# Kernel optimization log

Measured on AMD Instinct MI355X. Metric: run time of the kernel, lower is better.

## Reference

```python
import jax, jax.numpy as jnp
import numpy as np

H = 1024      # hidden_size
I = 2 * H     # intermediate_size (expand_factor=2)
N = 16        # ssm_state_size
K = 4         # conv_kernel
BATCH = 2
SEQ = 2048


def setup_inputs() -> dict:
    key = jax.random.key(0)
    k = jax.random.split(key, 6)
    x = jax.random.normal(k[0], (BATCH, SEQ, H), dtype=jnp.float32)
    # nn.Linear default init ~ U(-1/sqrt(fan_in), 1/sqrt(fan_in)); scale is fine for a reference
    W_in = jax.random.normal(k[1], (2 * I, H), dtype=jnp.float32) / np.sqrt(H)
    conv_w = jax.random.normal(k[2], (I, 1, K), dtype=jnp.float32) / np.sqrt(K)
    W_x = jax.random.normal(k[3], (2 * N + 1, I), dtype=jnp.float32) / np.sqrt(I)
    A_log = jax.random.normal(k[4], (I, N), dtype=jnp.float32)
    D = jnp.ones((I,), dtype=jnp.float32)
    W_out = jax.random.normal(k[5], (H, I), dtype=jnp.float32) / np.sqrt(I)
    return {"x": x, "W_in": W_in, "conv_w": conv_w, "W_x": W_x,
            "A_log": A_log, "D": D, "W_out": W_out}


def reference(x, W_in, conv_w, W_x, A_log, D, W_out):
    xz = jnp.einsum('bsh,ih->bsi', x, W_in)
    xp, z = jnp.split(xz, 2, axis=-1)
    # depthwise causal conv1d: pad left K-1 (torch pads both sides then slices [:S])
    xc = jax.lax.conv_general_dilated(
        xp.transpose(0, 2, 1),           # (B, I, S)
        conv_w,                          # (I, 1, K) = OIH with groups=I
        window_strides=(1,),
        padding=[(K - 1, 0)],
        feature_group_count=I,
        dimension_numbers=('NCH', 'OIH', 'NCH'),
    ).transpose(0, 2, 1)                 # (B, S, I)
    xc = jax.nn.silu(xc)
    # x_proj -> delta (1), B (N), C (N)
    xproj = jnp.einsum('bsi,pi->bsp', xc, W_x)   # (B,S,2N+1)
    delta = jax.nn.softplus(xproj[..., :1])       # (B,S,1)
    Bmat = xproj[..., 1:1 + N]                    # (B,S,N)
    Cmat = xproj[..., 1 + N:]                     # (B,S,N)
    A = -jnp.exp(A_log)                           # (I,N)
    # decay/states broadcast-reduce: (B,S,I,N) intermediates reduced over N
    decay = jnp.exp(delta[..., None] * A[None, None])            # (B,S,I,N)
    states = xc[..., None] * Bmat[:, :, None, :] * decay          # (B,S,I,N)
    y = jnp.sum(states * Cmat[:, :, None, :], axis=-1)            # (B,S,I)
    y = y + xc * D[None, None, :]
    return jnp.einsum('bsi,hi->bsh', y * jax.nn.silu(z), W_out)
```

## Files before the change

kernel.cpp:

```cpp
#include <hip/hip_runtime.h>

#define LOG2E 1.4426950408889634f

__device__ __forceinline__ float b2f(unsigned short u) {
    unsigned int v = ((unsigned int)u) << 16;
    return __builtin_bit_cast(float, v);
}
__device__ __forceinline__ unsigned short f2b(float f) {
    unsigned int u = __builtin_bit_cast(unsigned int, f);
    u += 0x7fffu + ((u >> 16) & 1u);
    return (unsigned short)(u >> 16);
}
__device__ __forceinline__ float fexp(float x) {
    return __builtin_amdgcn_exp2f(x * LOG2E);
}
__device__ __forceinline__ float silu_f(float x) {
    return x * __builtin_amdgcn_rcpf(1.0f + fexp(-x));
}

typedef const __attribute__((address_space(1))) unsigned int* gas_t;
typedef __attribute__((address_space(3))) unsigned int* las_t;
__device__ __forceinline__ void gl2lds16(const unsigned short* g, unsigned short* l) {
    __builtin_amdgcn_global_load_lds((gas_t)(const void*)g, (las_t)(void*)l, 16, 0, 0);
}

__global__ __launch_bounds__(256) void cvt_all_k(const float* __restrict__ x,
                                                 const float* __restrict__ W_in,
                                                 const float* __restrict__ W_out,
                                                 const float* __restrict__ W_x,
                                                 unsigned short* __restrict__ xb,
                                                 unsigned short* __restrict__ wib,
                                                 unsigned short* __restrict__ wob,
                                                 unsigned short* __restrict__ wxb) {
    int b = blockIdx.x;
    const float* src;
    unsigned short* dst;
    if (b < 4096)       { src = x;     dst = xb;  }
    else if (b < 8192)  { src = W_in;  dst = wib; b -= 4096; }
    else if (b < 10240) { src = W_out; dst = wob; b -= 8192; }
    else                { src = W_x;   dst = wxb; b -= 10240; }
    int i = b * 256 + threadIdx.x;
    float4 v = ((const float4*)src)[i];
    *(ushort4*)(dst + (size_t)i * 4) = make_ushort4(f2b(v.x), f2b(v.y), f2b(v.z), f2b(v.w));
}

typedef __bf16 bf16x8 __attribute__((ext_vector_type(8)));
typedef float  fx4    __attribute__((ext_vector_type(4)));
typedef int    ix4    __attribute__((ext_vector_type(4)));
union FragU { ix4 i; bf16x8 b; };

template <bool OUT_BF16>
__global__ __launch_bounds__(256) void gemm_bt(const unsigned short* __restrict__ A,
                                               const unsigned short* __restrict__ B,
                                               void* __restrict__ C, int N, int K) {
    __shared__ __align__(16) unsigned short sA[128 * 64];
    __shared__ __align__(16) unsigned short sB[128 * 64];
    const int tid  = threadIdx.x;
    const int lane = tid & 63, wave = tid >> 6;
    const int bm = blockIdx.y * 128, bn = blockIdx.x * 128;
    const int wm = (wave >> 1) * 64, wn = (wave & 1) * 64;
    const int row16 = lane & 15, quad = lane >> 4;
    const int srow = lane >> 3;
    const int sc16 = (lane & 7) ^ srow;
    const unsigned short* gA = A + (size_t)(bm + wave * 32 + srow) * K + sc16 * 8;
    const unsigned short* gB = B + (size_t)(bn + wave * 32 + srow) * K + sc16 * 8;
    unsigned short* lA = sA + (wave * 4) * 512;
    unsigned short* lB = sB + (wave * 4) * 512;
    fx4 acc[4][4] = {};

    for (int kt = 0; kt < K; kt += 64) {
#pragma unroll
        for (int it = 0; it < 4; ++it) {
            gl2lds16(gA + (size_t)it * 8 * K + kt, lA + it * 512);
            gl2lds16(gB + (size_t)it * 8 * K + kt, lB + it * 512);
        }
        __syncthreads();
#pragma unroll
        for (int kk = 0; kk < 64; kk += 32) {
            FragU af[4], bf[4];
#pragma unroll
            for (int t = 0; t < 4; ++t) {
                int ra = wm + t * 16 + row16;
                af[t].i = *(const ix4*)(sA + ra * 64 + ((quad + (kk >> 3)) ^ (ra & 7)) * 8);
            }
#pragma unroll
            for (int t = 0; t < 4; ++t) {
                int rb = wn + t * 16 + row16;
                bf[t].i = *(const ix4*)(sB + rb * 64 + ((quad + (kk >> 3)) ^ (rb & 7)) * 8);
            }
#pragma unroll
            for (int tm = 0; tm < 4; ++tm)
#pragma unroll
                for (int tn = 0; tn < 4; ++tn)
                    acc[tm][tn] = __builtin_amdgcn_mfma_f32_16x16x32_bf16(
                        af[tm].b, bf[tn].b, acc[tm][tn], 0, 0, 0);
        }
        __syncthreads();
    }
#pragma unroll
    for (int tm = 0; tm < 4; ++tm) {
        int row0 = bm + wm + tm * 16 + quad * 4;
#pragma unroll
        for (int tn = 0; tn < 4; ++tn) {
            int col = bn + wn + tn * 16 + row16;
#pragma unroll
            for (int r = 0; r < 4; ++r) {
                float v = acc[tm][tn][r];
                if (OUT_BF16)
                    ((unsigned short*)C)[(size_t)(row0 + r) * N + col] = f2b(v);
                else
                    ((float*)C)[(size_t)(row0 + r) * N + col] = v;
            }
        }
    }
}

__global__ __launch_bounds__(256) void gemm_bt_n64(const unsigned short* __restrict__ A,
                                                   const unsigned short* __restrict__ B,
                                                   float* __restrict__ C, int N, int K) {
    __shared__ __align__(16) unsigned short sA[128 * 64];
    __shared__ __align__(16) unsigned short sB[64 * 64];
    const int tid  = threadIdx.x;
    const int lane = tid & 63, wave = tid >> 6;
    const int bm = blockIdx.y * 128, bn = blockIdx.x * 64;
    const int wm = wave * 32;
    const int row16 = lane & 15, quad = lane >> 4;
    const int srow = lane >> 3;
    const int sc16 = (lane & 7) ^ srow;
    const unsigned short* gA = A + (size_t)(bm + wave * 32 + srow) * K + sc16 * 8;
    const unsigned short* gB = B + (size_t)(bn + wave * 16 + srow) * K + sc16 * 8;
    unsigned short* lA = sA + (wave * 4) * 512;
    unsigned short* lB = sB + (wave * 2) * 512;
    fx4 acc[2][4] = {};

    for (int kt = 0; kt < K; kt += 64) {
#pragma unroll
        for (int it = 0; it < 4; ++it)
            gl2lds16(gA + (size_t)it * 8 * K + kt, lA + it * 512);
#pragma unroll
        for (int it = 0; it < 2; ++it)
            gl2lds16(gB + (size_t)it * 8 * K + kt, lB + it * 512);
        __syncthreads();
#pragma unroll
        for (int kk = 0; kk < 64; kk += 32) {
            FragU af[2], bf[4];
#pragma unroll
            for (int t = 0; t < 2; ++t) {
                int ra = wm + t * 16 + row16;
                af[t].i = *(const ix4*)(sA + ra * 64 + ((quad + (kk >> 3)) ^ (ra & 7)) * 8);
            }
#pragma unroll
            for (int t = 0; t < 4; ++t) {
                int rb = t * 16 + row16;
                bf[t].i = *(const ix4*)(sB + rb * 64 + ((quad + (kk >> 3)) ^ (rb & 7)) * 8);
            }
#pragma unroll
            for (int tm = 0; tm < 2; ++tm)
#pragma unroll
                for (int tn = 0; tn < 4; ++tn)
                    acc[tm][tn] = __builtin_amdgcn_mfma_f32_16x16x32_bf16(
                        af[tm].b, bf[tn].b, acc[tm][tn], 0, 0, 0);
        }
        __syncthreads();
    }
#pragma unroll
    for (int tm = 0; tm < 2; ++tm) {
        int row0 = bm + wm + tm * 16 + quad * 4;
#pragma unroll
        for (int tn = 0; tn < 4; ++tn) {
            int col = bn + tn * 16 + row16;
#pragma unroll
            for (int r = 0; r < 4; ++r)
                C[(size_t)(row0 + r) * N + col] = acc[tm][tn][r];
        }
    }
}

__global__ __launch_bounds__(256) void conv_silu_k(const unsigned short* __restrict__ xz,
                                                   const float* __restrict__ cw,
                                                   unsigned short* __restrict__ xcb) {
    const int ti = threadIdx.x & 31, tm = threadIdx.x >> 5;
    const int i0 = blockIdx.x * 256 + ti * 8;
    const int m  = blockIdx.y * 8 + tm;
    const int s  = m & 2047;
    float w[8][4];
    const float4* cw4 = (const float4*)cw;
#pragma unroll
    for (int j = 0; j < 8; ++j) {
        float4 t = cw4[i0 + j];
        w[j][0] = t.x; w[j][1] = t.y; w[j][2] = t.z; w[j][3] = t.w;
    }
    float acc[8] = {0, 0, 0, 0, 0, 0, 0, 0};
#pragma unroll
    for (int k = 0; k < 4; ++k) {
        int sr = s - 3 + k;
        if (sr >= 0) {
            const unsigned short* p = xz + (size_t)(m - 3 + k) * 4096 + i0;
            ushort4 a = *(const ushort4*)p;
            ushort4 b = *(const ushort4*)(p + 4);
            float v[8] = {b2f(a.x), b2f(a.y), b2f(a.z), b2f(a.w),
                          b2f(b.x), b2f(b.y), b2f(b.z), b2f(b.w)};
#pragma unroll
            for (int j = 0; j < 8; ++j) acc[j] += v[j] * w[j][k];
        }
    }
    unsigned short* qb = xcb + (size_t)m * 2048 + i0;
    *(ushort4*)qb       = make_ushort4(f2b(silu_f(acc[0])), f2b(silu_f(acc[1])),
                                       f2b(silu_f(acc[2])), f2b(silu_f(acc[3])));
    *(ushort4*)(qb + 4) = make_ushort4(f2b(silu_f(acc[4])), f2b(silu_f(acc[5])),
                                       f2b(silu_f(acc[6])), f2b(silu_f(acc[7])));
}

__global__ __launch_bounds__(256) void xproj_mfma(const unsigned short* __restrict__ xcb,
                                                  const unsigned short* __restrict__ wxb,
                                                  float* __restrict__ dg) {
    __shared__ float sX[4][16][49];
    const int tid = threadIdx.x;
    const int lane = tid & 63, wave = tid >> 6;
    const int row16 = lane & 15, quad = lane >> 4;
    const int m0 = blockIdx.x * 16;
    fx4 acc[3] = {};
    const unsigned short* ap = xcb + (size_t)(m0 + row16) * 2048 + wave * 512 + quad * 8;
    const unsigned short* bp = wxb + (size_t)row16 * 2048 + wave * 512 + quad * 8;
#pragma unroll 4
    for (int kk = 0; kk < 512; kk += 32) {
        FragU a, b0, b1, b2;
        a.i  = *(const ix4*)(ap + kk);
        b0.i = *(const ix4*)(bp + kk);
        b1.i = *(const ix4*)(bp + 16 * 2048 + kk);
        b2.i = *(const ix4*)(bp + 32 * 2048 + kk);
        acc[0] = __builtin_amdgcn_mfma_f32_16x16x32_bf16(a.b, b0.b, acc[0], 0, 0, 0);
        acc[1] = __builtin_amdgcn_mfma_f32_16x16x32_bf16(a.b, b1.b, acc[1], 0, 0, 0);
        acc[2] = __builtin_amdgcn_mfma_f32_16x16x32_bf16(a.b, b2.b, acc[2], 0, 0, 0);
    }
#pragma unroll
    for (int t = 0; t < 3; ++t)
#pragma unroll
        for (int r = 0; r < 4; ++r)
            sX[wave][quad * 4 + r][t * 16 + row16] = acc[t][r];
    __syncthreads();
    for (int idx = tid; idx < 272; idx += 256) {
        int rr = idx / 17, q = idx - rr * 17;
        float o;
        if (q == 0) {
            float v = sX[0][rr][0] + sX[1][rr][0] + sX[2][rr][0] + sX[3][rr][0];
            o = (v > 20.f) ? v : log1pf(fexp(v));
        } else {
            float bs = sX[0][rr][q]      + sX[1][rr][q]      + sX[2][rr][q]      + sX[3][rr][q];
            float cs = sX[0][rr][q + 16] + sX[1][rr][q + 16] + sX[2][rr][q + 16] + sX[3][rr][q + 16];
            o = bs * cs;
        }
        dg[(size_t)(m0 + rr) * 17 + q] = o;
    }
}

__global__ __launch_bounds__(256) void ssm_pw_k(const unsigned short* __restrict__ xz,
                                                const unsigned short* __restrict__ xcb,
                                                const float* __restrict__ dg,
                                                const float* __restrict__ Alog,
                                                const float* __restrict__ Dv,
                                                unsigned short* __restrict__ y2) {
    __shared__ float sa[64 * 19];
    __shared__ float sdg[32 * 17];
    const int tid = threadIdx.x;
    const int bi = blockIdx.x, bm = blockIdx.y;
    for (int t = tid; t < 1024; t += 256) {
        float a = Alog[bi * 1024 + t];
        int il = t >> 4, n = t & 15;
        sa[il * 19 + n] = -fexp(a) * LOG2E;
    }
    for (int t = tid; t < 544; t += 256) sdg[t] = dg[(size_t)bm * 32 * 17 + t];
    __syncthreads();
    const int t_i = tid & 7, t_m = tid >> 3;
    const int m  = bm * 32 + t_m;
    const int i0 = bi * 64 + t_i * 8;
    const float delta = sdg[t_m * 17];
    float G[16];
#pragma unroll
    for (int n = 0; n < 16; ++n) G[n] = sdg[t_m * 17 + 1 + n];
    const unsigned short* xcp = xcb + (size_t)m * 2048 + i0;
    ushort4 xu0 = *(const ushort4*)xcp, xu1 = *(const ushort4*)(xcp + 4);
    const unsigned short* zp = xz + (size_t)m * 4096 + 2048 + i0;
    ushort4 zu0 = *(const ushort4*)zp, zu1 = *(const ushort4*)(zp + 4);
    float4 d0 = *(const float4*)(Dv + i0), d1 = *(const float4*)(Dv + i0 + 4);
    float xcv[8] = {b2f(xu0.x), b2f(xu0.y), b2f(xu0.z), b2f(xu0.w),
                    b2f(xu1.x), b2f(xu1.y), b2f(xu1.z), b2f(xu1.w)};
    float zv[8]  = {b2f(zu0.x), b2f(zu0.y), b2f(zu0.z), b2f(zu0.w),
                    b2f(zu1.x), b2f(zu1.y), b2f(zu1.z), b2f(zu1.w)};
    float dv[8]  = {d0.x, d0.y, d0.z, d0.w, d1.x, d1.y, d1.z, d1.w};
    unsigned short outv[8];
#pragma unroll
    for (int ii = 0; ii < 8; ++ii) {
        const float* ap = sa + (t_i * 8 + ii) * 19;
        float ssum = 0.f;
#pragma unroll
        for (int n = 0; n < 16; ++n)
            ssum += G[n] * __builtin_amdgcn_exp2f(delta * ap[n]);
        float y = xcv[ii] * (dv[ii] + ssum);
        outv[ii] = f2b(y * silu_f(zv[ii]));
    }
    unsigned short* q = y2 + (size_t)m * 2048 + i0;
    *(ushort4*)q       = make_ushort4(outv[0], outv[1], outv[2], outv[3]);
    *(ushort4*)(q + 4) = make_ushort4(outv[4], outv[5], outv[6], outv[7]);
}

extern "C" void kernel_launch(void* const* d_in, const int* in_sizes, int n_in,
                              void* d_out, int out_size, void* d_ws, size_t ws_size,
                              hipStream_t stream) {
    const float* x      = (const float*)d_in[0];
    const float* W_in   = (const float*)d_in[1];
    const float* conv_w = (const float*)d_in[2];
    const float* W_x    = (const float*)d_in[3];
    const float* A_log  = (const float*)d_in[4];
    const float* Dvec   = (const float*)d_in[5];
    const float* W_out  = (const float*)d_in[6];

    char* ws = (char*)d_ws;
    unsigned short* xb  = (unsigned short*)(ws);
    unsigned short* wib = (unsigned short*)(ws + 8388608);
    unsigned short* wob = (unsigned short*)(ws + 16777216);
    unsigned short* xz  = (unsigned short*)(ws + 20971520);
    float*          dgp = (float*)        (ws + 54525952);
    unsigned short* y2  = (unsigned short*)(ws + 54804480);
    unsigned short* xcb = (unsigned short*)(ws + 71581696);
    unsigned short* wxb = (unsigned short*)(ws + 88358912);

    cvt_all_k<<<10306, 256, 0, stream>>>(x, W_in, W_out, W_x, xb, wib, wob, wxb);
    gemm_bt<true><<<dim3(32, 32), 256, 0, stream>>>(xb, wib, xz, 4096, 1024);
    conv_silu_k<<<dim3(8, 512), 256, 0, stream>>>(xz, conv_w, xcb);
    xproj_mfma<<<256, 256, 0, stream>>>(xcb, wxb, dgp);
    ssm_pw_k<<<dim3(32, 128), 256, 0, stream>>>(xz, xcb, dgp, A_log, Dvec, y2);
    gemm_bt_n64<<<dim3(16, 32), 256, 0, stream>>>(y2, wob, (float*)d_out, 1024, 2048);
}
```

Before: 233.1 us.

## Fuse conv+silu, x_proj and SSM pointwise into one kernel via LDS

Merges the three middle kernels into one block-per-16-rows kernel that keeps the conv/silu output in swizzled shared memory, runs the x_proj MFMA from LDS, and computes the SSM pointwise output directly. This removes the global round trips for xc and the delta/G buffer and two kernel launches. In exchange, each block now recomputes exp(A_log) for all 2048 channels, and only 256 blocks with 64KB+ of LDS each run, which reduces parallelism and occupancy in the exp-heavy SSM stage.

```diff
diff --git a/kernel.cpp b/kernel.cpp
--- a/kernel.cpp
+++ b/kernel.cpp
@@ -176,68 +176,74 @@
     }
 }
 
-__global__ __launch_bounds__(256) void conv_silu_k(const unsigned short* __restrict__ xz,
+__global__ __launch_bounds__(256) void fused_mid_k(const unsigned short* __restrict__ xz,
                                                    const float* __restrict__ cw,
-                                                   unsigned short* __restrict__ xcb) {
-    const int ti = threadIdx.x & 31, tm = threadIdx.x >> 5;
-    const int i0 = blockIdx.x * 256 + ti * 8;
-    const int m  = blockIdx.y * 8 + tm;
-    const int s  = m & 2047;
-    float w[8][4];
-    const float4* cw4 = (const float4*)cw;
-#pragma unroll
-    for (int j = 0; j < 8; ++j) {
-        float4 t = cw4[i0 + j];
-        w[j][0] = t.x; w[j][1] = t.y; w[j][2] = t.z; w[j][3] = t.w;
-    }
-    float acc[8] = {0, 0, 0, 0, 0, 0, 0, 0};
-#pragma unroll
-    for (int k = 0; k < 4; ++k) {
-        int sr = s - 3 + k;
-        if (sr >= 0) {
-            const unsigned short* p = xz + (size_t)(m - 3 + k) * 4096 + i0;
-            ushort4 a = *(const ushort4*)p;
-            ushort4 b = *(const ushort4*)(p + 4);
-            float v[8] = {b2f(a.x), b2f(a.y), b2f(a.z), b2f(a.w),
-                          b2f(b.x), b2f(b.y), b2f(b.z), b2f(b.w)};
-#pragma unroll
-            for (int j = 0; j < 8; ++j) acc[j] += v[j] * w[j][k];
-        }
-    }
-    unsigned short* qb = xcb + (size_t)m * 2048 + i0;
-    *(ushort4*)qb       = make_ushort4(f2b(silu_f(acc[0])), f2b(silu_f(acc[1])),
-                                       f2b(silu_f(acc[2])), f2b(silu_f(acc[3])));
-    *(ushort4*)(qb + 4) = make_ushort4(f2b(silu_f(acc[4])), f2b(silu_f(acc[5])),
-                                       f2b(silu_f(acc[6])), f2b(silu_f(acc[7])));
-}
-
-__global__ __launch_bounds__(256) void xproj_mfma(const unsigned short* __restrict__ xcb,
-                                                  const unsigned short* __restrict__ wxb,
-                                                  float* __restrict__ dg) {
+                                                   const unsigned short* __restrict__ wxb,
+                                                   const float* __restrict__ Alog,
+                                                   const float* __restrict__ Dv,
+                                                   unsigned short* __restrict__ y2) {
+    __shared__ __align__(16) unsigned short sxc[16 * 2048];
     __shared__ float sX[4][16][49];
-    const int tid = threadIdx.x;
+    __shared__ float sdg[16 * 17];
+    const int tid  = threadIdx.x;
     const int lane = tid & 63, wave = tid >> 6;
     const int row16 = lane & 15, quad = lane >> 4;
     const int m0 = blockIdx.x * 16;
-    fx4 acc[3] = {};
-    const unsigned short* ap = xcb + (size_t)(m0 + row16) * 2048 + wave * 512 + quad * 8;
-    const unsigned short* bp = wxb + (size_t)row16 * 2048 + wave * 512 + quad * 8;
+
+    {
+        const float4* cw4 = (const float4*)cw;
+        float w[8][4];
+#pragma unroll
+        for (int c = 0; c < 8; ++c) {
+            float4 t4 = cw4[tid * 8 + c];
+            w[c][0] = t4.x; w[c][1] = t4.y; w[c][2] = t4.z; w[c][3] = t4.w;
+        }
+        for (int j = 0; j < 16; ++j) {
+            const int m = m0 + j, s = m & 2047;
+            float acc[8] = {0, 0, 0, 0, 0, 0, 0, 0};
+#pragma unroll
+            for (int k = 0; k < 4; ++k) {
+                if (s - 3 + k >= 0) {
+                    const unsigned short* p = xz + (size_t)(m - 3 + k) * 4096 + tid * 8;
+                    ushort4 a = *(const ushort4*)p;
+                    ushort4 b = *(const ushort4*)(p + 4);
+                    float v[8] = {b2f(a.x), b2f(a.y), b2f(a.z), b2f(a.w),
+                                  b2f(b.x), b2f(b.y), b2f(b.z), b2f(b.w)};
+#pragma unroll
+                    for (int c = 0; c < 8; ++c) acc[c] += v[c] * w[c][k];
+                }
+            }
+            unsigned short* q = sxc + j * 2048 + ((tid ^ (j & 7)) * 8);
+            *(ushort4*)q       = make_ushort4(f2b(silu_f(acc[0])), f2b(silu_f(acc[1])),
+                                              f2b(silu_f(acc[2])), f2b(silu_f(acc[3])));
+            *(ushort4*)(q + 4) = make_ushort4(f2b(silu_f(acc[4])), f2b(silu_f(acc[5])),
+                                              f2b(silu_f(acc[6])), f2b(silu_f(acc[7])));
+        }
+    }
+    __syncthreads();
+
+    {
+        fx4 acc[3] = {};
+        const unsigned short* bp = wxb + (size_t)row16 * 2048 + wave * 512 + quad * 8;
+        const int cbase = wave * 64 + quad;
 #pragma unroll 4
-    for (int kk = 0; kk < 512; kk += 32) {
-        FragU a, b0, b1, b2;
-        a.i  = *(const ix4*)(ap + kk);
-        b0.i = *(const ix4*)(bp + kk);
-        b1.i = *(const ix4*)(bp + 16 * 2048 + kk);
-        b2.i = *(const ix4*)(bp + 32 * 2048 + kk);
-        acc[0] = __builtin_amdgcn_mfma_f32_16x16x32_bf16(a.b, b0.b, acc[0], 0, 0, 0);
-        acc[1] = __builtin_amdgcn_mfma_f32_16x16x32_bf16(a.b, b1.b, acc[1], 0, 0, 0);
-        acc[2] = __builtin_amdgcn_mfma_f32_16x16x32_bf16(a.b, b2.b, acc[2], 0, 0, 0);
-    }
-#pragma unroll
-    for (int t = 0; t < 3; ++t)
-#pragma unroll
-        for (int r = 0; r < 4; ++r)
-            sX[wave][quad * 4 + r][t * 16 + row16] = acc[t][r];
+        for (int kk = 0; kk < 512; kk += 32) {
+            FragU a, b0, b1, b2;
+            int c16 = cbase + (kk >> 3);
+            a.i  = *(const ix4*)(sxc + row16 * 2048 + ((c16 ^ (row16 & 7)) * 8));
+            b0.i = *(const ix4*)(bp + kk);
+            b1.i = *(const ix4*)(bp + 16 * 2048 + kk);
+            b2.i = *(const ix4*)(bp + 32 * 2048 + kk);
+            acc[0] = __builtin_amdgcn_mfma_f32_16x16x32_bf16(a.b, b0.b, acc[0], 0, 0, 0);
+            acc[1] = __builtin_amdgcn_mfma_f32_16x16x32_bf16(a.b, b1.b, acc[1], 0, 0, 0);
+            acc[2] = __builtin_amdgcn_mfma_f32_16x16x32_bf16(a.b, b2.b, acc[2], 0, 0, 0);
+        }
+#pragma unroll
+        for (int t = 0; t < 3; ++t)
+#pragma unroll
+            for (int r = 0; r < 4; ++r)
+                sX[wave][quad * 4 + r][t * 16 + row16] = acc[t][r];
+    }
     __syncthreads();
     for (int idx = tid; idx < 272; idx += 256) {
         int rr = idx / 17, q = idx - rr * 17;
@@ -250,58 +256,52 @@
             float cs = sX[0][rr][q + 16] + sX[1][rr][q + 16] + sX[2][rr][q + 16] + sX[3][rr][q + 16];
             o = bs * cs;
         }
-        dg[(size_t)(m0 + rr) * 17 + q] = o;
-    }
-}
-
-__global__ __launch_bounds__(256) void ssm_pw_k(const unsigned short* __restrict__ xz,
-                                                const unsigned short* __restrict__ xcb,
-                                                const float* __restrict__ dg,
-                                                const float* __restrict__ Alog,
-                                                const float* __restrict__ Dv,
-                                                unsigned short* __restrict__ y2) {
-    __shared__ float sa[64 * 19];
-    __shared__ float sdg[32 * 17];
-    const int tid = threadIdx.x;
-    const int bi = blockIdx.x, bm = blockIdx.y;
-    for (int t = tid; t < 1024; t += 256) {
-        float a = Alog[bi * 1024 + t];
-        int il = t >> 4, n = t & 15;
-        sa[il * 19 + n] = -fexp(a) * LOG2E;
-    }
-    for (int t = tid; t < 544; t += 256) sdg[t] = dg[(size_t)bm * 32 * 17 + t];
+        sdg[rr * 17 + q] = o;
+    }
     __syncthreads();
-    const int t_i = tid & 7, t_m = tid >> 3;
-    const int m  = bm * 32 + t_m;
-    const int i0 = bi * 64 + t_i * 8;
-    const float delta = sdg[t_m * 17];
-    float G[16];
-#pragma unroll
-    for (int n = 0; n < 16; ++n) G[n] = sdg[t_m * 17 + 1 + n];
-    const unsigned short* xcp = xcb + (size_t)m * 2048 + i0;
-    ushort4 xu0 = *(const ushort4*)xcp, xu1 = *(const ushort4*)(xcp + 4);
-    const unsigned short* zp = xz + (size_t)m * 4096 + 2048 + i0;
-    ushort4 zu0 = *(const ushort4*)zp, zu1 = *(const ushort4*)(zp + 4);
-    float4 d0 = *(const float4*)(Dv + i0), d1 = *(const float4*)(Dv + i0 + 4);
-    float xcv[8] = {b2f(xu0.x), b2f(xu0.y), b2f(xu0.z), b2f(xu0.w),
-                    b2f(xu1.x), b2f(xu1.y), b2f(xu1.z), b2f(xu1.w)};
-    float zv[8]  = {b2f(zu0.x), b2f(zu0.y), b2f(zu0.z), b2f(zu0.w),
-                    b2f(zu1.x), b2f(zu1.y), b2f(zu1.z), b2f(zu1.w)};
-    float dv[8]  = {d0.x, d0.y, d0.z, d0.w, d1.x, d1.y, d1.z, d1.w};
-    unsigned short outv[8];
-#pragma unroll
-    for (int ii = 0; ii < 8; ++ii) {
-        const float* ap = sa + (t_i * 8 + ii) * 19;
-        float ssum = 0.f;
-#pragma unroll
-        for (int n = 0; n < 16; ++n)
-            ssum += G[n] * __builtin_amdgcn_exp2f(delta * ap[n]);
-        float y = xcv[ii] * (dv[ii] + ssum);
-        outv[ii] = f2b(y * silu_f(zv[ii]));
-    }
-    unsigned short* q = y2 + (size_t)m * 2048 + i0;
-    *(ushort4*)q       = make_ushort4(outv[0], outv[1], outv[2], outv[3]);
-    *(ushort4*)(q + 4) = make_ushort4(outv[4], outv[5], outv[6], outv[7]);
+
+#pragma unroll 1
+    for (int p = 0; p < 2; ++p) {
+        const int ch0 = p * 1024 + tid * 4;
+        float a2[4][16];
+#pragma unroll
+        for (int c = 0; c < 4; ++c) {
+            const float4* ar = (const float4*)(Alog + (size_t)(ch0 + c) * 16);
+#pragma unroll
+            for (int n4 = 0; n4 < 4; ++n4) {
+                float4 t4 = ar[n4];
+                a2[c][n4 * 4 + 0] = -fexp(t4.x) * LOG2E;
+                a2[c][n4 * 4 + 1] = -fexp(t4.y) * LOG2E;
+                a2[c][n4 * 4 + 2] = -fexp(t4.z) * LOG2E;
+                a2[c][n4 * 4 + 3] = -fexp(t4.w) * LOG2E;
+            }
+        }
+        float4 dvv = *(const float4*)(Dv + ch0);
+        float dv[4] = {dvv.x, dvv.y, dvv.z, dvv.w};
+        const int c16 = ch0 >> 3, sub = ch0 & 7;
+        for (int j = 0; j < 16; ++j) {
+            const int m = m0 + j;
+            float delta = sdg[j * 17];
+            float Gr[16];
+#pragma unroll
+            for (int n = 0; n < 16; ++n) Gr[n] = sdg[j * 17 + 1 + n];
+            ushort4 xu = *(const ushort4*)(sxc + j * 2048 + ((c16 ^ (j & 7)) * 8) + sub);
+            ushort4 zu = *(const ushort4*)(xz + (size_t)m * 4096 + 2048 + ch0);
+            float xcv[4] = {b2f(xu.x), b2f(xu.y), b2f(xu.z), b2f(xu.w)};
+            float zv[4]  = {b2f(zu.x), b2f(zu.y), b2f(zu.z), b2f(zu.w)};
+            unsigned short ov[4];
+#pragma unroll
+            for (int c = 0; c < 4; ++c) {
+                float ssum = 0.f;
+#pragma unroll
+                for (int n = 0; n < 16; ++n)
+                    ssum += Gr[n] * __builtin_amdgcn_exp2f(delta * a2[c][n]);
+                float y = xcv[c] * (dv[c] + ssum);
+                ov[c] = f2b(y * silu_f(zv[c]));
+            }
+            *(ushort4*)(y2 + (size_t)m * 2048 + ch0) = make_ushort4(ov[0], ov[1], ov[2], ov[3]);
+        }
+    }
 }
 
 extern "C" void kernel_launch(void* const* d_in, const int* in_sizes, int n_in,
@@ -320,15 +320,11 @@
     unsigned short* wib = (unsigned short*)(ws + 8388608);
     unsigned short* wob = (unsigned short*)(ws + 16777216);
     unsigned short* xz  = (unsigned short*)(ws + 20971520);
-    float*          dgp = (float*)        (ws + 54525952);
-    unsigned short* y2  = (unsigned short*)(ws + 54804480);
-    unsigned short* xcb = (unsigned short*)(ws + 71581696);
-    unsigned short* wxb = (unsigned short*)(ws + 88358912);
+    unsigned short* y2  = (unsigned short*)(ws + 54525952);
+    unsigned short* wxb = (unsigned short*)(ws + 71303168);
 
     cvt_all_k<<<10306, 256, 0, stream>>>(x, W_in, W_out, W_x, xb, wib, wob, wxb);
     gemm_bt<true><<<dim3(32, 32), 256, 0, stream>>>(xb, wib, xz, 4096, 1024);
-    conv_silu_k<<<dim3(8, 512), 256, 0, stream>>>(xz, conv_w, xcb);
-    xproj_mfma<<<256, 256, 0, stream>>>(xcb, wxb, dgp);
-    ssm_pw_k<<<dim3(32, 128), 256, 0, stream>>>(xz, xcb, dgp, A_log, Dvec, y2);
+    fused_mid_k<<<256, 256, 0, stream>>>(xz, conv_w, wxb, A_log, Dvec, y2);
     gemm_bt_n64<<<dim3(16, 32), 256, 0, stream>>>(y2, wob, (float*)d_out, 1024, 2048);
 }
```

After: 217.9 us. 1.07x faster.
